# Performance work log

Measured on AMD Instinct MI355X. Metric: run time of the kernel, lower is better.

## Reference

```python
import jax, jax.numpy as jnp
from jax import lax
import numpy as np

BIG = jnp.float32(1e6)  # 'no feature in this column' sentinel distance


def setup_inputs() -> dict:
    key = jax.random.key(0)
    k1, k2 = jax.random.split(key)
    # Binary segmentation masks in {0,1}; surf() only uses astype(bool), i.e. != 0.
    pred = (jax.random.uniform(k1, (512, 512)) > 0.5).astype(jnp.float32)
    gt = (jax.random.uniform(k2, (512, 512)) > 0.5).astype(jnp.float32)
    return {"pred": pred, "gt": gt}


def _erode(x):
    # scipy binary_erosion with connectivity-1 (cross) structure, border_value=0:
    # pixel survives iff it and its 4 neighbors are all True (out-of-bounds = False).
    p = jnp.pad(x, 1, constant_values=False)
    return x & p[:-2, 1:-1] & p[2:, 1:-1] & p[1:-1, :-2] & p[1:-1, 2:]


def _edt(feat):
    # Exact Euclidean distance from every pixel to the nearest True pixel of `feat`.
    # Equals scipy distance_transform_edt(~feat) in the original code.
    H, W = feat.shape
    # --- pass 1: per-column 1D distance |r - k| to nearest feature (two sweeps) ---
    def sweep(carry, row):
        c = jnp.where(row, jnp.float32(0.0), carry + jnp.float32(1.0))
        return c, c
    init = jnp.full((W,), BIG, dtype=jnp.float32)
    _, df = lax.scan(sweep, init, feat)          # distance to nearest feature above
    _, db = lax.scan(sweep, init, feat[::-1])    # ... below
    g = jnp.minimum(df, db[::-1])                # [H, W] vertical distance
    g2 = g * g
    # --- pass 2: row-wise min-plus over column offsets (exact, separable) ---
    j = jnp.arange(W, dtype=jnp.float32)
    delta2 = (j[:, None] - j[None, :]) ** 2      # [W(c), W(j)]
    # D[r, c] = min_j ( g2[r, j] + (c - j)^2 )   -> [H, W, W] intermediate
    d2 = jnp.min(g2[:, None, :] + delta2[None, :, :], axis=-1)
    return jnp.sqrt(d2)


def reference(pred, gt):
    p = pred != 0
    g = gt != 0
    # Surface = mask minus its erosion
    S = p & ~_erode(p)
    Sprime = g & ~_erode(g)
    dta = _edt(S)       # distance field to pred surface (== edt(~S))
    dtb = _edt(Sprime)  # distance field to gt surface
    sm = S.astype(jnp.float32)
    spm = Sprime.astype(jnp.float32)
    # mean of concat(dta[Sprime], dtb[S]) without dynamic shapes
    num = jnp.sum(dta * spm) + jnp.sum(dtb * sm)
    den = jnp.sum(spm) + jnp.sum(sm)
    return num / den
```

## Files before the change

### kernel.cpp

```cpp
#include <hip/hip_runtime.h>

#define HH 512
#define WW 512
#define NPIX (HH*WW)

__global__ __launch_bounds__(256) void surf_kernel(
        const float* __restrict__ pred, const float* __restrict__ gt,
        unsigned char* __restrict__ mAB, unsigned int* __restrict__ ticket) {
    int idx4 = blockIdx.x * 256 + threadIdx.x;
    if (idx4 == 0) { *ticket = 0u; }
    if (idx4 >= NPIX / 4) return;
    int r  = idx4 >> 7;
    int c4 = (idx4 & 127) << 2;

    unsigned char bits[4] = {0, 0, 0, 0};
    const float* srcs[2] = { pred, gt };
    #pragma unroll
    for (int f = 0; f < 2; ++f) {
        const float* x = srcs[f];
        float4 v = ((const float4*)x)[idx4];
        float4 u = (r > 0)      ? ((const float4*)x)[idx4 - 128] : make_float4(0,0,0,0);
        float4 d = (r < HH - 1) ? ((const float4*)x)[idx4 + 128] : make_float4(0,0,0,0);
        float lS = (c4 > 0)        ? x[r * WW + c4 - 1] : 0.0f;
        float rS = (c4 + 4 < WW)   ? x[r * WW + c4 + 4] : 0.0f;
        float vv[4] = { v.x, v.y, v.z, v.w };
        float uu[4] = { u.x, u.y, u.z, u.w };
        float dd[4] = { d.x, d.y, d.z, d.w };
        #pragma unroll
        for (int e = 0; e < 4; ++e) {
            int c = c4 + e;
            bool ctr = vv[e] != 0.0f;
            bool up  = (r > 0)      && (uu[e] != 0.0f);
            bool dn  = (r < HH - 1) && (dd[e] != 0.0f);
            bool lf  = (c > 0)      && ((e == 0 ? lS : vv[e - 1]) != 0.0f);
            bool rt  = (c < WW - 1) && ((e == 3 ? rS : vv[e + 1]) != 0.0f);
            if (ctr && !(up && dn && lf && rt)) bits[e] |= (1 << f);
        }
    }
    uchar4 out;
    out.x = bits[0]; out.y = bits[1]; out.z = bits[2]; out.w = bits[3];
    ((uchar4*)mAB)[idx4] = out;
}

__global__ __launch_bounds__(512) void edt_kernel(
        const unsigned char* __restrict__ mAB,
        double* __restrict__ partials, unsigned int* __restrict__ ticket,
        float* __restrict__ out) {
    __shared__ float2 s2[WW];
    __shared__ double lred[16];
    __shared__ int winner;
    int r = blockIdx.x;
    int c = threadIdx.x;

    unsigned int own = mAB[r * WW + c];
    bool fa = (own & 1u) != 0u;
    bool fb = (own & 2u) != 0u;

    int foundA = fa ? 0 : -1;
    int foundB = fb ? 0 : -1;
    for (int kb = 1; kb < HH && (foundA < 0 || foundB < 0); kb += 4) {
        unsigned int mu[4], md[4];
        #pragma unroll
        for (int i = 0; i < 4; ++i) {
            int ku = kb + i;
            int ru = r - ku, rd = r + ku;
            mu[i] = (ru >= 0) ? (unsigned int)mAB[ru * WW + c] : 0u;
            md[i] = (rd < HH) ? (unsigned int)mAB[rd * WW + c] : 0u;
        }
        #pragma unroll
        for (int i = 0; i < 4; ++i) {
            unsigned int hit = mu[i] | md[i];
            if (foundA < 0 && (hit & 1u)) foundA = kb + i;
            if (foundB < 0 && (hit & 2u)) foundB = kb + i;
        }
    }
    float sent = 1e6f + (float)((r + 1 < HH - r) ? (r + 1) : (HH - r));
    float ga = (foundA >= 0) ? (float)foundA : sent;
    float gb = (foundB >= 0) ? (float)foundB : sent;
    s2[c] = make_float2(ga * ga, gb * gb);
    __syncthreads();

    float2 o2 = s2[c];
    float besta = o2.x, bestb = o2.y;
    for (int kb = 1; kb < WW; kb += 4) {
        float kk2 = (float)(kb * kb);
        if (kk2 >= besta && kk2 >= bestb) break;
        #pragma unroll
        for (int i = 0; i < 4; ++i) {
            int k = kb + i;
            float k2 = (float)(k * k);
            int cl = c - k, cr = c + k;
            if (cl >= 0) {
                float2 g = s2[cl];
                besta = fminf(besta, g.x + k2);
                bestb = fminf(bestb, g.y + k2);
            }
            if (cr < WW) {
                float2 g = s2[cr];
                besta = fminf(besta, g.x + k2);
                bestb = fminf(bestb, g.y + k2);
            }
        }
    }

    float wA = fa ? 1.0f : 0.0f;
    float wB = fb ? 1.0f : 0.0f;
    double lnum = (double)(sqrtf(besta) * wB + sqrtf(bestb) * wA);
    double lden = (double)(wA + wB);
    for (int off = 32; off > 0; off >>= 1) {
        lnum += __shfl_down(lnum, off, 64);
        lden += __shfl_down(lden, off, 64);
    }
    int wv = c >> 6;
    if ((c & 63) == 0) { lred[wv] = lnum; lred[8 + wv] = lden; }
    __syncthreads();
    if (c == 0) {
        double n = 0.0, d = 0.0;
        #pragma unroll
        for (int i = 0; i < 8; ++i) { n += lred[i]; d += lred[8 + i]; }
        partials[2 * r]     = n;
        partials[2 * r + 1] = d;
        __threadfence();
        unsigned int old = atomicAdd(ticket, 1u);
        winner = (old == HH - 1) ? 1 : 0;
    }
    __syncthreads();

    if (winner) {
        __threadfence();
        double n = partials[2 * c];
        double d = partials[2 * c + 1];
        for (int off = 32; off > 0; off >>= 1) {
            n += __shfl_down(n, off, 64);
            d += __shfl_down(d, off, 64);
        }
        if ((c & 63) == 0) { lred[c >> 6] = n; lred[8 + (c >> 6)] = d; }
        __syncthreads();
        if (c == 0) {
            double nn = 0.0, dd = 0.0;
            #pragma unroll
            for (int i = 0; i < 8; ++i) { nn += lred[i]; dd += lred[8 + i]; }
            out[0] = (float)(nn / dd);
        }
    }
}

extern "C" void kernel_launch(void* const* d_in, const int* in_sizes, int n_in,
                              void* d_out, int out_size, void* d_ws, size_t ws_size,
                              hipStream_t stream) {
    const float* pred = (const float*)d_in[0];
    const float* gt   = (const float*)d_in[1];
    float* out = (float*)d_out;

    char* ws = (char*)d_ws;
    unsigned int* tick = (unsigned int*)ws;
    double* partials   = (double*)(ws + 256);
    unsigned char* mAB = (unsigned char*)(ws + 256 + 8192);

    surf_kernel<<<NPIX / 4 / 256, 256, 0, stream>>>(pred, gt, mAB, tick);
    edt_kernel<<<HH, 512, 0, stream>>>(mAB, partials, tick, out);
}
```

Measured before the change: 72.90 us.

## Fuse surface extraction and EDT into one cooperative kernel with grid sync

Merges the surface-mask kernel into the EDT kernel. Each 512-thread block first computes the surface bits for its own row, then a cooperative grid.sync() separates that phase from the distance phase. The launch becomes a single hipLaunchCooperativeKernel. This removes one kernel launch and the gap between the two kernels, at the cost of a grid-wide barrier, a residency requirement of 512 blocks, and scalar loads where the old code used float4 loads.

```diff
diff --git a/kernel.cpp b/kernel.cpp
--- a/kernel.cpp
+++ b/kernel.cpp
@@ -1,60 +1,44 @@
 #include <hip/hip_runtime.h>
+#include <hip/hip_cooperative_groups.h>
+
+namespace cg = cooperative_groups;
 
 #define HH 512
 #define WW 512
 #define NPIX (HH*WW)
 
-__global__ __launch_bounds__(256) void surf_kernel(
+__global__ __launch_bounds__(512, 4) void fused_kernel(
         const float* __restrict__ pred, const float* __restrict__ gt,
-        unsigned char* __restrict__ mAB, unsigned int* __restrict__ ticket) {
-    int idx4 = blockIdx.x * 256 + threadIdx.x;
-    if (idx4 == 0) { *ticket = 0u; }
-    if (idx4 >= NPIX / 4) return;
-    int r  = idx4 >> 7;
-    int c4 = (idx4 & 127) << 2;
-
-    unsigned char bits[4] = {0, 0, 0, 0};
-    const float* srcs[2] = { pred, gt };
-    #pragma unroll
-    for (int f = 0; f < 2; ++f) {
-        const float* x = srcs[f];
-        float4 v = ((const float4*)x)[idx4];
-        float4 u = (r > 0)      ? ((const float4*)x)[idx4 - 128] : make_float4(0,0,0,0);
-        float4 d = (r < HH - 1) ? ((const float4*)x)[idx4 + 128] : make_float4(0,0,0,0);
-        float lS = (c4 > 0)        ? x[r * WW + c4 - 1] : 0.0f;
-        float rS = (c4 + 4 < WW)   ? x[r * WW + c4 + 4] : 0.0f;
-        float vv[4] = { v.x, v.y, v.z, v.w };
-        float uu[4] = { u.x, u.y, u.z, u.w };
-        float dd[4] = { d.x, d.y, d.z, d.w };
-        #pragma unroll
-        for (int e = 0; e < 4; ++e) {
-            int c = c4 + e;
-            bool ctr = vv[e] != 0.0f;
-            bool up  = (r > 0)      && (uu[e] != 0.0f);
-            bool dn  = (r < HH - 1) && (dd[e] != 0.0f);
-            bool lf  = (c > 0)      && ((e == 0 ? lS : vv[e - 1]) != 0.0f);
-            bool rt  = (c < WW - 1) && ((e == 3 ? rS : vv[e + 1]) != 0.0f);
-            if (ctr && !(up && dn && lf && rt)) bits[e] |= (1 << f);
-        }
-    }
-    uchar4 out;
-    out.x = bits[0]; out.y = bits[1]; out.z = bits[2]; out.w = bits[3];
-    ((uchar4*)mAB)[idx4] = out;
-}
-
-__global__ __launch_bounds__(512) void edt_kernel(
-        const unsigned char* __restrict__ mAB,
+        unsigned char* __restrict__ mAB,
         double* __restrict__ partials, unsigned int* __restrict__ ticket,
         float* __restrict__ out) {
+    cg::grid_group grid = cg::this_grid();
     __shared__ float2 s2[WW];
     __shared__ double lred[16];
     __shared__ int winner;
+
     int r = blockIdx.x;
     int c = threadIdx.x;
+    int idx = r * WW + c;
+    if (idx == 0) *ticket = 0u;
 
-    unsigned int own = mAB[r * WW + c];
-    bool fa = (own & 1u) != 0u;
-    bool fb = (own & 2u) != 0u;
+    float pc_ = pred[idx];
+    float pu = (r > 0)      ? pred[idx - WW] : 0.0f;
+    float pd = (r < HH - 1) ? pred[idx + WW] : 0.0f;
+    float pl = (c > 0)      ? pred[idx - 1]  : 0.0f;
+    float pr = (c < WW - 1) ? pred[idx + 1]  : 0.0f;
+    float gc = gt[idx];
+    float gu = (r > 0)      ? gt[idx - WW] : 0.0f;
+    float gd = (r < HH - 1) ? gt[idx + WW] : 0.0f;
+    float gl = (c > 0)      ? gt[idx - 1]  : 0.0f;
+    float gr = (c < WW - 1) ? gt[idx + 1]  : 0.0f;
+    bool fa = (pc_ != 0.0f) &&
+              !((pu != 0.0f) && (pd != 0.0f) && (pl != 0.0f) && (pr != 0.0f));
+    bool fb = (gc != 0.0f) &&
+              !((gu != 0.0f) && (gd != 0.0f) && (gl != 0.0f) && (gr != 0.0f));
+    mAB[idx] = (unsigned char)((fa ? 1u : 0u) | (fb ? 2u : 0u));
+
+    grid.sync();
 
     int foundA = fa ? 0 : -1;
     int foundB = fb ? 0 : -1;
@@ -157,6 +141,8 @@
     double* partials   = (double*)(ws + 256);
     unsigned char* mAB = (unsigned char*)(ws + 256 + 8192);
 
-    surf_kernel<<<NPIX / 4 / 256, 256, 0, stream>>>(pred, gt, mAB, tick);
-    edt_kernel<<<HH, 512, 0, stream>>>(mAB, partials, tick, out);
+    void* args[] = { (void*)&pred, (void*)&gt, (void*)&mAB,
+                     (void*)&partials, (void*)&tick, (void*)&out };
+    hipLaunchCooperativeKernel((const void*)fused_kernel, dim3(HH), dim3(WW),
+                               args, 0, stream);
 }
```

Result: slower. 120.5 us (+65.2%).
